# Performance work log

Hardware: AMD Instinct MI355X
Metric: run time of the kernel (lower is better)

The kernel has to match this reference:

```python
import jax, jax.numpy as jnp
import numpy as np

D = 100  # embedding_dim (hard-coded in the original module)


def _prelu(x, a):
    return jnp.where(x >= 0, x, a * x)


def setup_inputs() -> dict:
    key = jax.random.key(0)
    ks = jax.random.split(key, 12)
    B, S, L, R, V = 32, 50, 20, 16, 50000
    T = L * R  # tokens per sentence = len_max_sentence * n_routes
    return {
        "stories": jax.random.randint(ks[0], (B, S, T), 0, V),
        "queries": jax.random.randint(ks[1], (B, L), 0, V),
        "emb": 0.1 * jax.random.normal(ks[2], (V, D), dtype=jnp.float32),
        "in_mult": jnp.ones((T, D), dtype=jnp.float32),
        "q_mult": jnp.ones((L, D), dtype=jnp.float32),
        "keys": 0.1 * jax.random.normal(ks[3], (R, D), dtype=jnp.float32),
        "init_state": 0.1 * jax.random.normal(ks[4], (D,), dtype=jnp.float32),
        "U": 0.1 * jax.random.normal(ks[5], (R * D, D), dtype=jnp.float32),
        "Vw": 0.1 * jax.random.normal(ks[6], (R * D, R * D), dtype=jnp.float32),
        "Ww": 0.1 * jax.random.normal(ks[7], (R * D, R * D), dtype=jnp.float32),
        "Hw": 0.1 * jax.random.normal(ks[8], (D, D), dtype=jnp.float32),
        "Rw": 0.1 * jax.random.normal(ks[9], (V, D), dtype=jnp.float32),
        "alpha_in": jnp.ones((1,), dtype=jnp.float32),  # PReLU(init=1)
        "alpha_q": jnp.ones((1,), dtype=jnp.float32),
    }


def reference(stories, queries, emb, in_mult, q_mult, keys, init_state,
              U, Vw, Ww, Hw, Rw, alpha_in, alpha_q):
    B, S, T = stories.shape
    R = keys.shape[0]
    emb0 = emb.at[0].set(0.0)  # padding_idx=0 row is zero
    # stories -> [B,S,T,D] -> route-sum -> [B,S,R,D]
    x = emb0[stories] * in_mult
    x = x.reshape(B, S, R, T // R, D).sum(axis=3)
    # V(keys.flatten()) is constant across timesteps
    v_keys = (keys.reshape(-1) @ Vw.T).reshape(R, D)
    state0 = jnp.tile(init_state[None, None, :], (B, 1, 1))  # [B,1,D]

    def step(state, sent):  # state [B,1,D], sent [B,R,D]
        gate = jax.nn.sigmoid(sent * state + sent * keys)
        u = (state.reshape(B, D) @ U.T).reshape(B, R, D)
        w = (sent.reshape(B, R * D) @ Ww.T).reshape(B, R, D)
        cand = _prelu(u + v_keys + w, alpha_in)
        # null-sentence mask: zero out positions where gate == sigmoid(0) = 0.5
        mask = jax.lax.stop_gradient(jnp.where(gate == 0.5, 0.0, 1.0))
        state = state + (cand * gate * mask).sum(axis=1, keepdims=True)
        # torch.norm over singleton dim=1 (= elementwise abs), kept faithful
        state = state / jnp.sqrt(jnp.sum(state * state, axis=1, keepdims=True))
        return state, None

    state, _ = jax.lax.scan(step, state0, jnp.swapaxes(x, 0, 1))

    q = (emb0[queries] * q_mult).sum(axis=1, keepdims=True)  # [B,1,D]
    h = _prelu(q + (state.reshape(B, D) @ Hw.T).reshape(B, 1, D), alpha_q)
    return h.reshape(B, D) @ Rw.T  # [B, vocab]
```

## Files before the change

kernel.cpp:

```cpp
#include <hip/hip_runtime.h>
#include <cstddef>
#include <cstdint>

#define B_  32
#define S_  50
#define L_  20
#define R_  16
#define D_  100
#define V_  50000
#define T_  320
#define RD_ 1600
#define BS_ 1600
#define NG_ 25
#define NP_ 16

typedef float v4f __attribute__((ext_vector_type(4)));
typedef unsigned short u16;
#define NTL(p)   __builtin_nontemporal_load((const v4f*)(p))
#define NTLS(p)  __builtin_nontemporal_load((const float*)(p))

__device__ __forceinline__ void bsplit(float a, unsigned& h, unsigned& l) {
  const unsigned bits = __float_as_uint(a);
  const unsigned hb = bits & 0xffff0000u;
  h = hb >> 16;
  l = __float_as_uint(a - __uint_as_float(hb)) >> 16;
}

__device__ __forceinline__ void bsplit4(float4 a, uint2& h, uint2& l) {
  unsigned h0,h1,h2,h3,l0,l1,l2,l3;
  bsplit(a.x, h0, l0); bsplit(a.y, h1, l1);
  bsplit(a.z, h2, l2); bsplit(a.w, h3, l3);
  h.x = h0 | (h1 << 16); h.y = h2 | (h3 << 16);
  l.x = l0 | (l1 << 16); l.y = l2 | (l3 << 16);
}

__global__ __launch_bounds__(512) void setup_kernel(
    const int* __restrict__ stories, const float* __restrict__ emb,
    const float* __restrict__ in_mult, const float* __restrict__ U,
    const float* __restrict__ Vw, const float* __restrict__ keys,
    const float* __restrict__ init_state, const float* __restrict__ Ww,
    float* __restrict__ x,
    u16* __restrict__ wh, u16* __restrict__ wl,
    float* __restrict__ table, float* __restrict__ vk, float* __restrict__ u0)
{
  const int blk = blockIdx.x, tid = threadIdx.x;
  if (blk < 1600) {
    __shared__ int toks[T_];
    const int* st = stories + (size_t)blk * T_;
    if (tid < T_) toks[tid] = st[tid];
    __syncthreads();
    if (tid < 400) {
      const int j4 = tid * 4;
      const int r  = j4 / D_;
      const int d4 = j4 - r * D_;
      float4 acc = make_float4(0.f, 0.f, 0.f, 0.f);
      #pragma unroll
      for (int l = 0; l < 20; ++l) {
        const int t = r * 20 + l;
        const int tok = toks[t];
        if (tok != 0) {
          float4 e = *(const float4*)&emb[(size_t)tok * D_ + d4];
          float4 m = *(const float4*)&in_mult[(size_t)t * D_ + d4];
          acc.x += e.x * m.x; acc.y += e.y * m.y;
          acc.z += e.z * m.z; acc.w += e.w * m.w;
        }
      }
      *(float4*)&x[(size_t)blk * RD_ + j4] = acc;
    }
  } else if (blk < 2000) {
    const int qq = blk - 1600;
    const int g = qq >> 4, p = qq & 15;
    const float s0 = (p & 1) ? -1.f : 1.f;
    const float s1 = (p & 2) ? -1.f : 1.f;
    const float s2 = (p & 4) ? -1.f : 1.f;
    const float s3 = (p & 8) ? -1.f : 1.f;
    if (tid < 400) {
      const int d  = tid >> 2;
      const int r0 = (tid & 3) * 4;
      float t[4];
      #pragma unroll
      for (int ri = 0; ri < 4; ++ri) {
        const int orig = (r0 + ri) * D_ + d;
        const float* ur = &U[(size_t)orig * D_ + 4 * g];
        t[ri] = s0*ur[0] + s1*ur[1] + s2*ur[2] + s3*ur[3];
      }
      *(float4*)&table[((size_t)(g * NP_ + p)) * RD_ + tid * 4] =
          make_float4(t[0], t[1], t[2], t[3]);
    }
  } else if (blk < 2200) {
    const int wave = tid >> 6, lane = tid & 63;
    const int jp = (blk - 2000) * 8 + wave;
    const int orig = (jp & 15) * D_ + (jp >> 4);
    float acc = 0.f;
    for (int k = lane; k < RD_; k += 64)
      acc += keys[k] * Vw[(size_t)orig * RD_ + k];
    #pragma unroll
    for (int off = 32; off > 0; off >>= 1) acc += __shfl_down(acc, off);
    if (lane == 0) vk[jp] = acc;
  } else if (blk < 2400) {
    const int wave = tid >> 6, lane = tid & 63;
    const int jp = (blk - 2200) * 8 + wave;
    const int orig = (jp & 15) * D_ + (jp >> 4);
    const float* Ur = U + (size_t)orig * D_;
    float acc = Ur[lane] * init_state[lane];
    if (lane < 36) acc += Ur[64 + lane] * init_state[64 + lane];
    #pragma unroll
    for (int off = 32; off > 0; off >>= 1) acc += __shfl_down(acc, off);
    if (lane == 0) u0[jp] = acc;
  } else {
    const int g   = (blk - 2400) * 512 + tid;
    const int row = g / 200;
    const int c8  = (g - row * 200) * 8;
    const int orig = (row & 15) * D_ + (row >> 4);
    const float* src = &Ww[(size_t)orig * RD_ + c8];
    float4 a0 = *(const float4*)src;
    float4 a1 = *(const float4*)(src + 4);
    uint2 h0, l0, h1, l1;
    bsplit4(a0, h0, l0);
    bsplit4(a1, h1, l1);
    uint4 hv = make_uint4(h0.x, h0.y, h1.x, h1.y);
    uint4 lv = make_uint4(l0.x, l0.y, l1.x, l1.y);
    *(uint4*)&wh[(size_t)row * RD_ + c8] = hv;
    *(uint4*)&wl[(size_t)row * RD_ + c8] = lv;
  }
}

typedef const __attribute__((address_space(1))) unsigned GAu;
typedef __attribute__((address_space(3))) unsigned LDSu;
#define GLL(SRC, DST) __builtin_amdgcn_global_load_lds((GAu*)(SRC), (LDSu*)(DST), 16, 0, 0)

__device__ __forceinline__ void mfma16(v4f& d, v4f a, v4f b) {
  asm("v_mfma_f32_16x16x32_bf16 %0, %1, %2, %0" : "+v"(d) : "v"(a), "v"(b));
}

__global__ __launch_bounds__(512) void gemm_mfma_kernel(
    const float* __restrict__ A,
    const u16* __restrict__ wh, const u16* __restrict__ wl,
    float* __restrict__ C)
{
  __shared__ __align__(16) char smem[2][4][8192];
  const int tid = threadIdx.x;
  const int lane = tid & 63, wid = tid >> 6;
  const int bm = blockIdx.y * 128, bn = blockIdx.x * 128;

  const int brow = wid * 16 + (lane >> 2);
  const int bkb  = (lane & 3) * 16;
  int rb = bn + brow; if (rb > 1599) rb = 1599;
  const int srcB = rb * 3200 + bkb;
  const int ldsB = wid * 1024;
  const char* gwh = (const char*)wh;
  const char* gwl = (const char*)wl;

  int arow[2], awofs[2];
  const int akseg = tid & 7;
  #pragma unroll
  for (int i = 0; i < 2; ++i) {
    const int r = i * 64 + (tid >> 3);
    int ra = bm + r; if (ra > 1599) ra = 1599;
    arow[i] = ra;
    awofs[i] = r * 64 + akseg * 8;
  }

  const int wm = wid >> 2, wn = wid & 3;
  const int r15 = lane & 15, q = lane >> 4;
  const int aoff = (wm * 64 + r15) * 64 + q * 16;
  const int boff = (wn * 32 + r15) * 64 + q * 16;

  v4f acc[4][2];
  #pragma unroll
  for (int i = 0; i < 4; ++i)
    #pragma unroll
    for (int j = 0; j < 2; ++j) acc[i][j] = (v4f)(0.f);

  auto stageB = [&](int buf, int kt) {
    const int kb = kt * 64;
    GLL(gwh + srcB + kb, &smem[buf][2][ldsB]);
    GLL(gwl + srcB + kb, &smem[buf][3][ldsB]);
  };

  float4 a4[2];
  #pragma unroll
  for (int i = 0; i < 2; ++i)
    a4[i] = *(const float4*)&A[(size_t)arow[i] * RD_ + akseg * 4];
  stageB(0, 0);
  #pragma unroll
  for (int i = 0; i < 2; ++i) {
    uint2 h, l; bsplit4(a4[i], h, l);
    *(uint2*)&smem[0][0][awofs[i]] = h;
    *(uint2*)&smem[0][1][awofs[i]] = l;
  }
  __syncthreads();

  for (int kt = 0; kt < 50; ++kt) {
    const int cur = kt & 1;
    if (kt < 49) {
      stageB(cur ^ 1, kt + 1);
      #pragma unroll
      for (int i = 0; i < 2; ++i)
        a4[i] = *(const float4*)&A[(size_t)arow[i] * RD_ + (kt + 1) * 32 + akseg * 4];
    }
    const char* s0 = &smem[cur][0][0];
    v4f ah[4], al[4], bh[2], bl[2];
    #pragma unroll
    for (int t = 0; t < 4; ++t) {
      ah[t] = *(const v4f*)(s0 +         aoff + t * 1024);
      al[t] = *(const v4f*)(s0 +  8192 + aoff + t * 1024);
    }
    #pragma unroll
    for (int t = 0; t < 2; ++t) {
      bh[t] = *(const v4f*)(s0 + 16384 + boff + t * 1024);
      bl[t] = *(const v4f*)(s0 + 24576 + boff + t * 1024);
    }
    #pragma unroll
    for (int im = 0; im < 4; ++im)
      #pragma unroll
      for (int in = 0; in < 2; ++in) {
        mfma16(acc[im][in], ah[im], bh[in]);
        mfma16(acc[im][in], ah[im], bl[in]);
        mfma16(acc[im][in], al[im], bh[in]);
      }
    if (kt < 49) {
      const int nxt = cur ^ 1;
      #pragma unroll
      for (int i = 0; i < 2; ++i) {
        uint2 h, l; bsplit4(a4[i], h, l);
        *(uint2*)&smem[nxt][0][awofs[i]] = h;
        *(uint2*)&smem[nxt][1][awofs[i]] = l;
      }
    }
    __syncthreads();
  }

  const int mb  = bm + wm * 64 + q * 4;
  const int nbq = bn + wn * 32 + r15;
  #pragma unroll
  for (int im = 0; im < 4; ++im) {
    #pragma unroll
    for (int in = 0; in < 2; ++in) {
      const int n = nbq + in * 16;
      const int m0 = mb + im * 16;
      if (n < 1600) {
        #pragma unroll
        for (int r = 0; r < 4; ++r)
          if (m0 + r < 1600)
            C[(size_t)(m0 + r) * RD_ + n] = acc[im][in][r];
      }
    }
  }
}

__global__ __launch_bounds__(448, 2) void scan_kernel(
    const float* __restrict__ x,
    const float* __restrict__ Wall,
    const float* __restrict__ table,
    const float* __restrict__ u0,
    const float* __restrict__ vkeys,
    const float* __restrict__ keys,
    const float* __restrict__ init_state,
    const float* __restrict__ alpha_in_p,
    const int*   __restrict__ queries,
    const float* __restrict__ emb,
    const float* __restrict__ q_mult,
    const float* __restrict__ Hw,
    const float* __restrict__ alpha_q_p,
    float* __restrict__ h_g)
{
  const int b = blockIdx.x, tid = threadIdx.x;
  __shared__ __align__(16) float s_state[D_];
  __shared__ float s_hw[D_ * 101];
  __shared__ __align__(16) unsigned char s_sign[2][112];
  const float alpha = alpha_in_p[0];
  const bool active = (tid < 400);
  const int q4 = tid * 4;
  const int d  = tid >> 2;
  const int r0 = (tid & 3) * 4;
  int xo0 = 0, xo1 = 0, xo2 = 0, xo3 = 0;
  float kk0 = 0.f, kk1 = 0.f, kk2 = 0.f, kk3 = 0.f;
  float4 vv = make_float4(0.f, 0.f, 0.f, 0.f);
  float state_reg = 0.f;
  const float* xb = x    + (size_t)b * S_ * RD_;
  const float* wb = Wall + (size_t)b * S_ * RD_;
  float4 bx[5], bw[5];
  #pragma unroll
  for (int i = 0; i < 5; ++i) {
    bx[i] = make_float4(0.f, 0.f, 0.f, 0.f);
    bw[i] = make_float4(0.f, 0.f, 0.f, 0.f);
  }
  if (active) {
    xo0 = (r0 + 0) * D_ + d;  xo1 = (r0 + 1) * D_ + d;
    xo2 = (r0 + 2) * D_ + d;  xo3 = (r0 + 3) * D_ + d;
    kk0 = keys[xo0]; kk1 = keys[xo1]; kk2 = keys[xo2]; kk3 = keys[xo3];
    vv = *(const float4*)&vkeys[q4];
    state_reg = init_state[d];
    #pragma unroll
    for (int i = 0; i < 5; ++i) {
      const float* xr = xb + (size_t)i * RD_;
      bx[i].x = NTLS(xr + xo0); bx[i].y = NTLS(xr + xo1);
      bx[i].z = NTLS(xr + xo2); bx[i].w = NTLS(xr + xo3);
      v4f wv = NTL(&wb[(size_t)i * RD_ + q4]);
      bw[i] = make_float4(wv.x, wv.y, wv.z, wv.w);
    }
  }
  __syncthreads();

  for (int sg = 0; sg < S_; sg += 5) {
    #pragma unroll
    for (int i = 0; i < 5; ++i) {
      const int s = sg + i;
      if (active) {
        const float4 sent = bx[i], w = bw[i];
        const bool first = (s == 0);
        v4f tv[NG_];
        if (first) {
          tv[0] = *(const v4f*)&u0[q4];
        } else {
          const uint4* sp = (const uint4*)s_sign[s & 1];
          unsigned wd[25];
          uint4 s0v = sp[0]; wd[0]=s0v.x;  wd[1]=s0v.y;  wd[2]=s0v.z;  wd[3]=s0v.w;
          uint4 s1v = sp[1]; wd[4]=s1v.x;  wd[5]=s1v.y;  wd[6]=s1v.z;  wd[7]=s1v.w;
          uint4 s2v = sp[2]; wd[8]=s2v.x;  wd[9]=s2v.y;  wd[10]=s2v.z; wd[11]=s2v.w;
          uint4 s3v = sp[3]; wd[12]=s3v.x; wd[13]=s3v.y; wd[14]=s3v.z; wd[15]=s3v.w;
          uint4 s4v = sp[4]; wd[16]=s4v.x; wd[17]=s4v.y; wd[18]=s4v.z; wd[19]=s4v.w;
          uint4 s5v = sp[5]; wd[20]=s5v.x; wd[21]=s5v.y; wd[22]=s5v.z; wd[23]=s5v.w;
          uint4 s6v = sp[6]; wd[24]=s6v.x;
          #pragma unroll
          for (int g = 0; g < NG_; ++g) {
            const unsigned idx = (wd[g] * 0x01020408u) >> 24;
            tv[g] = *(const v4f*)&table[((size_t)(g * NP_) + idx) * RD_ + q4];
          }
        }
        __builtin_amdgcn_sched_barrier(0);
        if (s + 5 < S_) {
          const float* xr = xb + (size_t)(s + 5) * RD_;
          bx[i].x = NTLS(xr + xo0); bx[i].y = NTLS(xr + xo1);
          bx[i].z = NTLS(xr + xo2); bx[i].w = NTLS(xr + xo3);
          v4f wv = NTL(&wb[(size_t)(s + 5) * RD_ + q4]);
          bw[i] = make_float4(wv.x, wv.y, wv.z, wv.w);
        }
        const float sd = state_reg;
        float zx = sent.x * sd + sent.x * kk0;
        float zy = sent.y * sd + sent.y * kk1;
        float zz = sent.z * sd + sent.z * kk2;
        float zw = sent.w * sd + sent.w * kk3;
        float gx = 1.0f / (1.0f + expf(-zx));
        float gy = 1.0f / (1.0f + expf(-zy));
        float gz = 1.0f / (1.0f + expf(-zz));
        float gw = 1.0f / (1.0f + expf(-zw));
        v4f u = tv[0];
        if (!first) {
          #pragma unroll
          for (int g = 1; g < NG_; ++g) {
            u.x += tv[g].x; u.y += tv[g].y; u.z += tv[g].z; u.w += tv[g].w;
          }
        }
        float cx = u.x + vv.x + w.x; cx = cx >= 0.f ? cx : alpha * cx;
        float cy = u.y + vv.y + w.y; cy = cy >= 0.f ? cy : alpha * cy;
        float cz = u.z + vv.z + w.z; cz = cz >= 0.f ? cz : alpha * cz;
        float cw = u.w + vv.w + w.w; cw = cw >= 0.f ? cw : alpha * cw;
        float p  = ((gx == 0.5f) ? 0.f : cx * gx)
                 + ((gy == 0.5f) ? 0.f : cy * gy)
                 + ((gz == 0.5f) ? 0.f : cz * gz)
                 + ((gw == 0.5f) ? 0.f : cw * gw);
        p += __shfl_xor(p, 1);
        p += __shfl_xor(p, 2);
        float v = state_reg + p;
        state_reg = v / sqrtf(v * v);
        if ((tid & 3) == 0) s_sign[(s + 1) & 1][d] = (v < 0.f) ? 1 : 0;
      }
      __syncthreads();
    }
  }

  if (active && (tid & 3) == 0) s_state[d] = state_reg;
  __syncthreads();

  for (int f = tid; f < D_ * D_; f += 448) {
    const int row = f / D_, col = f - row * D_;
    s_hw[row * 101 + col] = Hw[f];
  }
  __syncthreads();
  if (tid < D_) {
    float q = 0.f;
    #pragma unroll
    for (int l = 0; l < L_; ++l) {
      const int tok = queries[b * L_ + l];
      if (tok != 0) q += emb[(size_t)tok * D_ + tid] * q_mult[l * D_ + tid];
    }
    float a = 0.f;
    #pragma unroll 4
    for (int k = 0; k < D_; ++k) a += s_state[k] * s_hw[tid * 101 + k];
    float h = q + a;
    const float aq = alpha_q_p[0];
    h = h >= 0.f ? h : aq * h;
    h_g[(size_t)b * D_ + tid] = h;
  }
}

__global__ __launch_bounds__(256) void out_kernel(
    const float* __restrict__ h_g, const float* __restrict__ Rw, float* __restrict__ out)
{
  __shared__ __align__(16) float sh[B_ * D_];
  __shared__ __align__(16) float sr[32 * D_];
  int tid = threadIdx.x;
  int v0 = blockIdx.x * 32;
  for (int i = tid; i < B_ * D_; i += 256) sh[i] = h_g[i];
  int nrows = V_ - v0; if (nrows > 32) nrows = 32;
  for (int i = tid; i < nrows * D_; i += 256) sr[i] = Rw[(size_t)v0 * D_ + i];
  __syncthreads();
  const float4* sh4 = (const float4*)sh;
  const float4* sr4 = (const float4*)sr;
  int tv = (tid & 15) * 2;
  int tb = (tid >> 4) * 2;
  float a00 = 0.f, a01 = 0.f, a10 = 0.f, a11 = 0.f;
  #pragma unroll
  for (int kc = 0; kc < 25; ++kc) {
    float4 h0 = sh4[tb * 25 + kc];
    float4 h1 = sh4[(tb + 1) * 25 + kc];
    float4 r0 = sr4[tv * 25 + kc];
    float4 r1 = sr4[(tv + 1) * 25 + kc];
    a00 += h0.x*r0.x + h0.y*r0.y + h0.z*r0.z + h0.w*r0.w;
    a01 += h0.x*r1.x + h0.y*r1.y + h0.z*r1.z + h0.w*r1.w;
    a10 += h1.x*r0.x + h1.y*r0.y + h1.z*r0.z + h1.w*r0.w;
    a11 += h1.x*r1.x + h1.y*r1.y + h1.z*r1.z + h1.w*r1.w;
  }
  if (tv < nrows) {
    out[(size_t)tb * V_ + v0 + tv] = a00;
    out[(size_t)(tb + 1) * V_ + v0 + tv] = a10;
  }
  if (tv + 1 < nrows) {
    out[(size_t)tb * V_ + v0 + tv + 1] = a01;
    out[(size_t)(tb + 1) * V_ + v0 + tv + 1] = a11;
  }
}

extern "C" void kernel_launch(void* const* d_in, const int* in_sizes, int n_in,
                              void* d_out, int out_size, void* d_ws, size_t ws_size,
                              hipStream_t stream) {
  const int*   stories    = (const int*)  d_in[0];
  const int*   queries    = (const int*)  d_in[1];
  const float* emb        = (const float*)d_in[2];
  const float* in_mult    = (const float*)d_in[3];
  const float* q_mult     = (const float*)d_in[4];
  const float* keys       = (const float*)d_in[5];
  const float* init_state = (const float*)d_in[6];
  const float* U          = (const float*)d_in[7];
  const float* Vw         = (const float*)d_in[8];
  const float* Ww         = (const float*)d_in[9];
  const float* Hw         = (const float*)d_in[10];
  const float* Rw         = (const float*)d_in[11];
  const float* alpha_in   = (const float*)d_in[12];
  const float* alpha_q    = (const float*)d_in[13];
  float* out = (float*)d_out;

  char* ws = (char*)d_ws;
  float* x     = (float*)(ws);
  float* Wall  = (float*)(ws + 10240000);
  float* table = (float*)(ws + 20480000);
  u16*   wwh   = (u16*)  (ws + 23040000);
  u16*   wwl   = (u16*)  (ws + 28160000);
  float* vk    = (float*)(ws + 33280000);
  float* u0    = (float*)(ws + 33286400);
  float* hbuf  = (float*)(ws + 33292800);

  setup_kernel<<<3025, 512, 0, stream>>>(stories, emb, in_mult, U, Vw, keys,
                                         init_state, Ww, x, wwh, wwl,
                                         table, vk, u0);
  gemm_mfma_kernel<<<dim3(13, 13), 512, 0, stream>>>(x, wwh, wwl, Wall);
  scan_kernel<<<B_, 448, 0, stream>>>(x, Wall, table, u0, vk, keys, init_state,
                                      alpha_in, queries, emb, q_mult, Hw, alpha_q,
                                      hbuf);
  out_kernel<<<(V_ + 31) / 32, 256, 0, stream>>>(hbuf, Rw, out);
}
```

Baseline: 372.2 us.

## Store route-summed inputs d-major and permute Ww columns to match

The setup kernel now writes the route-summed sentence tensor x in a d-major (d*16+r) layout instead of r-major, and permutes the Ww column order the same way when splitting it into bf16 hi/lo. The recurrent kernel can then fetch each thread's four sentence values with one vectorized 16-byte nontemporal load instead of four strided scalar loads. The cost is scattered scalar stores in setup, plus strided reads of Ww during the conversion.

```diff
diff --git a/kernel.cpp b/kernel.cpp
--- a/kernel.cpp
+++ b/kernel.cpp
@@ -17,7 +17,6 @@
 typedef float v4f __attribute__((ext_vector_type(4)));
 typedef unsigned short u16;
 #define NTL(p)   __builtin_nontemporal_load((const v4f*)(p))
-#define NTLS(p)  __builtin_nontemporal_load((const float*)(p))
 
 __device__ __forceinline__ void bsplit(float a, unsigned& h, unsigned& l) {
   const unsigned bits = __float_as_uint(a);
@@ -65,7 +64,11 @@
           acc.z += e.z * m.z; acc.w += e.w * m.w;
         }
       }
-      *(float4*)&x[(size_t)blk * RD_ + j4] = acc;
+      float* xo = x + (size_t)blk * RD_;
+      xo[(d4 + 0) * 16 + r] = acc.x;
+      xo[(d4 + 1) * 16 + r] = acc.y;
+      xo[(d4 + 2) * 16 + r] = acc.z;
+      xo[(d4 + 3) * 16 + r] = acc.w;
     }
   } else if (blk < 2000) {
     const int qq = blk - 1600;
@@ -110,18 +113,21 @@
   } else {
     const int g   = (blk - 2400) * 512 + tid;
     const int row = g / 200;
-    const int c8  = (g - row * 200) * 8;
+    const int rem = g - row * 200;
+    const int d   = rem % 100;
+    const int r0  = (rem / 100) * 8;
     const int orig = (row & 15) * D_ + (row >> 4);
-    const float* src = &Ww[(size_t)orig * RD_ + c8];
-    float4 a0 = *(const float4*)src;
-    float4 a1 = *(const float4*)(src + 4);
-    uint2 h0, l0, h1, l1;
-    bsplit4(a0, h0, l0);
-    bsplit4(a1, h1, l1);
-    uint4 hv = make_uint4(h0.x, h0.y, h1.x, h1.y);
-    uint4 lv = make_uint4(l0.x, l0.y, l1.x, l1.y);
-    *(uint4*)&wh[(size_t)row * RD_ + c8] = hv;
-    *(uint4*)&wl[(size_t)row * RD_ + c8] = lv;
+    const float* src = Ww + (size_t)orig * RD_;
+    unsigned h[8], l[8];
+    #pragma unroll
+    for (int i = 0; i < 8; ++i)
+      bsplit(src[(r0 + i) * D_ + d], h[i], l[i]);
+    uint4 hv = make_uint4(h[0]|(h[1]<<16), h[2]|(h[3]<<16),
+                          h[4]|(h[5]<<16), h[6]|(h[7]<<16));
+    uint4 lv = make_uint4(l[0]|(l[1]<<16), l[2]|(l[3]<<16),
+                          l[4]|(l[5]<<16), l[6]|(l[7]<<16));
+    *(uint4*)&wh[(size_t)row * RD_ + d * 16 + r0] = hv;
+    *(uint4*)&wl[(size_t)row * RD_ + d * 16 + r0] = lv;
   }
 }
 
@@ -274,7 +280,6 @@
   const int q4 = tid * 4;
   const int d  = tid >> 2;
   const int r0 = (tid & 3) * 4;
-  int xo0 = 0, xo1 = 0, xo2 = 0, xo3 = 0;
   float kk0 = 0.f, kk1 = 0.f, kk2 = 0.f, kk3 = 0.f;
   float4 vv = make_float4(0.f, 0.f, 0.f, 0.f);
   float state_reg = 0.f;
@@ -287,17 +292,17 @@
     bw[i] = make_float4(0.f, 0.f, 0.f, 0.f);
   }
   if (active) {
-    xo0 = (r0 + 0) * D_ + d;  xo1 = (r0 + 1) * D_ + d;
-    xo2 = (r0 + 2) * D_ + d;  xo3 = (r0 + 3) * D_ + d;
-    kk0 = keys[xo0]; kk1 = keys[xo1]; kk2 = keys[xo2]; kk3 = keys[xo3];
+    kk0 = keys[(r0 + 0) * D_ + d];
+    kk1 = keys[(r0 + 1) * D_ + d];
+    kk2 = keys[(r0 + 2) * D_ + d];
+    kk3 = keys[(r0 + 3) * D_ + d];
     vv = *(const float4*)&vkeys[q4];
     state_reg = init_state[d];
     #pragma unroll
     for (int i = 0; i < 5; ++i) {
-      const float* xr = xb + (size_t)i * RD_;
-      bx[i].x = NTLS(xr + xo0); bx[i].y = NTLS(xr + xo1);
-      bx[i].z = NTLS(xr + xo2); bx[i].w = NTLS(xr + xo3);
+      v4f xv = NTL(&xb[(size_t)i * RD_ + q4]);
       v4f wv = NTL(&wb[(size_t)i * RD_ + q4]);
+      bx[i] = make_float4(xv.x, xv.y, xv.z, xv.w);
       bw[i] = make_float4(wv.x, wv.y, wv.z, wv.w);
     }
   }
@@ -331,10 +336,9 @@
         }
         __builtin_amdgcn_sched_barrier(0);
         if (s + 5 < S_) {
-          const float* xr = xb + (size_t)(s + 5) * RD_;
-          bx[i].x = NTLS(xr + xo0); bx[i].y = NTLS(xr + xo1);
-          bx[i].z = NTLS(xr + xo2); bx[i].w = NTLS(xr + xo3);
+          v4f xv = NTL(&xb[(size_t)(s + 5) * RD_ + q4]);
           v4f wv = NTL(&wb[(size_t)(s + 5) * RD_ + q4]);
+          bx[i] = make_float4(xv.x, xv.y, xv.z, xv.w);
           bw[i] = make_float4(wv.x, wv.y, wv.z, wv.w);
         }
         const float sd = state_reg;
```

Result: faster. 364.9 us (-2.0%).
